# Kernel tuning notes

Hardware: AMD Instinct MI355X
Metric: run time of the kernel (lower is better)

Reference implementation:

```python
import jax, jax.numpy as jnp
import numpy as np

B, Lc, Le, H, V = 128, 512, 512, 512, 128
PAD_IDX = 0  # ignore_index for cross entropy


def _lstm_cell(x, h, c, Wih, Whh, bih, bhh):
    # PyTorch gate order: i, f, g, o
    gates = x @ Wih.T + h @ Whh.T + bih + bhh
    i, f, g, o = jnp.split(gates, 4, axis=-1)
    c_new = jax.nn.sigmoid(f) * c + jax.nn.sigmoid(i) * jnp.tanh(g)
    h_new = jax.nn.sigmoid(o) * jnp.tanh(c_new)
    return h_new, c_new


def setup_inputs() -> dict:
    key = jax.random.key(0)
    ks = jax.random.split(key, 16)
    s = 0.05  # weight init scale
    inp = {
        "C": jax.random.normal(ks[0], (B, Lc, V), jnp.float32),
        "C_pad": jax.random.randint(ks[1], (B, Lc), 0, 2, jnp.int32).at[:, 0].set(0),
        "E": jax.random.randint(ks[2], (B, Le), 0, V, jnp.int32),
        "E_emb": jax.random.normal(ks[3], (B, Le, V), jnp.float32),
        # encoder LSTM (input V -> hidden H)
        "enc_Wih": s * jax.random.normal(ks[4], (4 * H, V), jnp.float32),
        "enc_Whh": s * jax.random.normal(ks[5], (4 * H, H), jnp.float32),
        "enc_bih": jnp.zeros((4 * H,), jnp.float32),
        "enc_bhh": jnp.zeros((4 * H,), jnp.float32),
        # decoder LSTMCell (input V+H -> hidden H); input is concat([E_emb_t, V_prev])
        "dec_Wih": s * jax.random.normal(ks[6], (4 * H, V + H), jnp.float32),
        "dec_Whh": s * jax.random.normal(ks[7], (4 * H, H), jnp.float32),
        "dec_bih": jnp.zeros((4 * H,), jnp.float32),
        "dec_bhh": jnp.zeros((4 * H,), jnp.float32),
        # attention_proj: Linear(H, H, bias=False)
        "att_W": s * jax.random.normal(ks[8], (H, H), jnp.float32),
        # output_proj: Linear(2H, H)
        "out_W": s * jax.random.normal(ks[9], (H, 2 * H), jnp.float32),
        "out_b": jnp.zeros((H,), jnp.float32),
        # vocab_proj: Linear(H, V)
        "voc_W": s * jax.random.normal(ks[10], (V, H), jnp.float32),
        "voc_b": jnp.zeros((V,), jnp.float32),
    }
    return inp


def reference(C, C_pad, E, E_emb, enc_Wih, enc_Whh, enc_bih, enc_bhh,
              dec_Wih, dec_Whh, dec_bih, dec_bhh, att_W, out_W, out_b,
              voc_W, voc_b):
    Bv = C.shape[0]
    Hh = enc_Whh.shape[1]

    # ---- encoder LSTM over compressed input ----
    def enc_step(carry, x_t):
        h, c = carry
        h, c = _lstm_cell(x_t, h, c, enc_Wih, enc_Whh, enc_bih, enc_bhh)
        return (h, c), h

    h0 = jnp.zeros((Bv, Hh), C.dtype)
    (hT, cT), enc_hs = jax.lax.scan(enc_step, (h0, h0), jnp.swapaxes(C, 0, 1))
    enc_hs = jnp.swapaxes(enc_hs, 0, 1)  # (B, Lc, H)
    pad = C_pad.astype(bool)              # (B, Lc)

    # ---- decoder loop (training mode, teacher forcing) ----
    def dec_step(carry, e_t):
        h, c, Vprev = carry
        x = jnp.concatenate([e_t, Vprev], axis=1)  # (B, V+H)
        h, c = _lstm_cell(x, h, c, dec_Wih, dec_Whh, dec_bih, dec_bhh)
        q = h @ att_W.T                                    # (B, H)
        scores = jnp.einsum('blh,bh->bl', enc_hs, q)       # (B, Lc)
        scores = jnp.where(pad, -jnp.inf, scores)
        d = jax.nn.softmax(scores, axis=1)
        attn = jnp.einsum('bl,blh->bh', d, enc_hs)         # (B, H)
        U = jnp.concatenate([h, attn], axis=1)             # (B, 2H)
        Vnew = U @ out_W.T + out_b                         # (B, H)
        # dropout treated as identity (eval-mode determinism)
        logits = jnp.tanh(Vnew) @ voc_W.T + voc_b          # (B, V)
        return (h, c, Vnew), logits

    Vinit = jnp.zeros((Bv, Hh), C.dtype)
    _, logits = jax.lax.scan(dec_step, (hT, cT, Vinit),
                             jnp.swapaxes(E_emb[:, :-1], 0, 1))
    logits = jnp.swapaxes(logits, 0, 1)  # (B, Le-1, V)

    # ---- cross entropy with ignore_index=PAD_IDX ----
    targets = E[:, 1:].astype(jnp.int32)
    logp = jax.nn.log_softmax(logits, axis=-1)
    nll = -jnp.take_along_axis(logp, targets[..., None], axis=-1)[..., 0]
    mask = (targets != PAD_IDX).astype(nll.dtype)
    loss = jnp.sum(nll * mask) / jnp.maximum(jnp.sum(mask), 1.0)
    return loss
```

## Files before the change

kernel.cpp:

```cpp
#include <hip/hip_runtime.h>
#include <hip/hip_bf16.h>


#define NWG 256
#define NT  256

typedef unsigned short u16;
typedef unsigned int   u32;
typedef unsigned long long u64;
typedef __attribute__((ext_vector_type(4))) float f4;
typedef __attribute__((ext_vector_type(8))) short s8;

constexpr int Bv=128, Lc=512, Le=512, Hd=512, Vc=128;
constexpr int KE=640, KD=1152;
constexpr int CAP = 144;
constexpr int SPN = 24;

constexpr size_t O_WENC = 4096;
constexpr size_t O_WDEC = O_WENC + (size_t)2048*KE*2;
constexpr size_t O_WDF  = O_WDEC + (size_t)2048*KD*2;
constexpr size_t O_ATWT = O_WDF  + (size_t)2048*KD*2;
constexpr size_t O_OUTW = O_ATWT + (size_t)512*512*2;
constexpr size_t O_VOCW = O_OUTW + (size_t)512*1024*2;
constexpr size_t O_BE   = O_VOCW + (size_t)128*512*2;
constexpr size_t O_BD   = O_BE + 8192;
constexpr size_t O_BDF  = O_BD + 8192;
constexpr size_t O_H    = O_BDF + 8192;
constexpr size_t O_TNH  = O_H + (size_t)2*128*512*2;
constexpr size_t O_PFX  = O_TNH + (size_t)2*128*512*2;
constexpr size_t O_CNT  = O_PFX + (size_t)128*512*4;
constexpr size_t O_PMS  = O_CNT + 512;
constexpr size_t O_PACC = O_PMS + 2048;
constexpr size_t O_REC  = O_PACC + (size_t)256*512*2;
constexpr size_t O_LOSS = O_REC + (size_t)2*128*2*4*4;
constexpr size_t O_ENC  = O_LOSS + 256;
constexpr size_t O_PSP  = O_ENC + (size_t)128*512*512*2;

constexpr int SC       = CAP*1024;
constexpr int SM_BYTES = SC + 16384;

struct P {
  const float *C; const int *Cpad; const int *E; const float *Eemb;
  const float *eWih,*eWhh,*ebih,*ebhh;
  const float *dWih,*dWhh,*dbih,*dbhh;
  const float *attW,*outW,*outb,*vocW,*vocb;
  char* ws; float* out;
};

__device__ inline u16 f2bf(float x){
  u32 u = __float_as_uint(x);
  return (u16)((u + 0x7fffu + ((u>>16)&1u)) >> 16);
}
__device__ inline float bf2f(u16 b){ return __uint_as_float(((u32)b)<<16); }
__device__ inline float sigm(float x){ return 1.f/(1.f+expf(-x)); }
__device__ inline f4 MM(s8 a, s8 b, f4 c){
  return __builtin_amdgcn_mfma_f32_16x16x32_bf16(a, b, c, 0, 0, 0);
}
__device__ inline u64 ld64a(const void* p){
  return __hip_atomic_load((const u64*)p, __ATOMIC_RELAXED, __HIP_MEMORY_SCOPE_AGENT);
}
__device__ inline u32 ld32u(const void* p){
  return __hip_atomic_load((const u32*)p, __ATOMIC_RELAXED, __HIP_MEMORY_SCOPE_AGENT);
}
__device__ inline void st64a(void* p, u64 v){
  __hip_atomic_store((u64*)p, v, __ATOMIC_RELAXED, __HIP_MEMORY_SCOPE_AGENT);
}
__device__ inline void st32a(void* p, u32 v){
  __hip_atomic_store((u32*)p, v, __ATOMIC_RELAXED, __HIP_MEMORY_SCOPE_AGENT);
}
__device__ inline s8 ld16a(const void* p){
  union { u64 q[2]; s8 v; } u;
  u.q[0] = ld64a(p); u.q[1] = ld64a((const char*)p + 8);
  return u.v;
}
__device__ inline s8 cvt8(const float* p){
  f4 u = *(const f4*)p, v = *(const f4*)(p+4);
  s8 r;
  r[0]=(short)f2bf(u[0]); r[1]=(short)f2bf(u[1]); r[2]=(short)f2bf(u[2]); r[3]=(short)f2bf(u[3]);
  r[4]=(short)f2bf(v[0]); r[5]=(short)f2bf(v[1]); r[6]=(short)f2bf(v[2]); r[7]=(short)f2bf(v[3]);
  return r;
}
__device__ inline float wredmax(float v){
  #pragma unroll
  for (int m=32;m;m>>=1) v = fmaxf(v, __shfl_xor(v,m,64));
  return v;
}
__device__ inline float wredsum(float v){
  #pragma unroll
  for (int m=32;m;m>>=1) v += __shfl_xor(v,m,64);
  return v;
}

extern "C" __global__ void __launch_bounds__(NT,1) k_main(P p)
{
  extern __shared__ char sm[];
  const int wg = blockIdx.x, tid = threadIdx.x;
  const int gt = wg*NT + tid;
  const int rg = wg >> 5, cg = wg & 31;

  char* ws = p.ws;
  u32*  slotA = (u32*)ws;
  u32*  slotR = (u32*)(ws + 1024 + rg*128);
  u16*  wenc = (u16*)(ws + O_WENC);
  u16*  wdec = (u16*)(ws + O_WDEC);
  u16*  wdf  = (u16*)(ws + O_WDF);
  u16*  atwt = (u16*)(ws + O_ATWT);
  u16*  outw = (u16*)(ws + O_OUTW);
  u16*  vocw = (u16*)(ws + O_VOCW);
  float* be  = (float*)(ws + O_BE);
  float* bd  = (float*)(ws + O_BD);
  float* bdf = (float*)(ws + O_BDF);
  u16*  hbf  = (u16*)(ws + O_H);
  u16*  tnhb = (u16*)(ws + O_TNH);
  u32*  pfx  = (u32*)(ws + O_PFX);
  u32*  cntp = (u32*)(ws + O_CNT);
  u64*  pms  = (u64*)(ws + O_PMS);
  u16*  pacc16 = (u16*)(ws + O_PACC);
  float* rec = (float*)(ws + O_REC);
  float* losp= (float*)(ws + O_LOSS);
  u16*  encc = (u16*)(ws + O_ENC);
  u16*  spl  = (u16*)(ws + O_PSP) + (size_t)wg*SPN*Hd;

  u32 genA = 0, genG = 0;
  auto GBall = [&](){
    genA++;
    __syncthreads();
    if (tid == 0){
      __builtin_amdgcn_fence(__ATOMIC_RELEASE, "agent");
      st32a(slotA + wg, genA);
    }
    if (tid < 64){
      bool done = false;
      while (!done){
        u32 v0 = ld32u(slotA + tid);
        u32 v1 = ld32u(slotA + 64 + tid);
        u32 v2 = ld32u(slotA + 128 + tid);
        u32 v3 = ld32u(slotA + 192 + tid);
        done = __all((v0>=genA)&&(v1>=genA)&&(v2>=genA)&&(v3>=genA));
        if (!done) __builtin_amdgcn_s_sleep(4);
      }
      __builtin_amdgcn_fence(__ATOMIC_ACQUIRE, "agent");
    }
    __syncthreads();
  };
  auto RGB = [&](){
    genG++;
    __syncthreads();
    if (tid == 0) st32a(slotR + cg, genG);
    if (tid < 64){
      bool done = false;
      while (!done){
        u32 v = ld32u(slotR + (tid & 31));
        done = __all(v >= genG);
        if (!done) __builtin_amdgcn_s_sleep(2);
      }
      __builtin_amdgcn_fence(__ATOMIC_ACQUIRE, "workgroup");
    }
    __syncthreads();
  };

  for (int i = gt; i < 2048*KE; i += NWG*NT){
    int row = i / KE, k = i - row*KE;
    float v = (k < 128) ? p.eWih[row*128 + k] : p.eWhh[row*512 + (k-128)];
    wenc[i] = f2bf(v);
  }
  for (int i = gt; i < 2048*KD; i += NWG*NT){
    int row = i / KD, k = i - row*KD;
    float v = (k < 640) ? p.dWih[row*640 + k] : p.dWhh[row*512 + (k-640)];
    wdec[i] = f2bf(v);
  }
  for (int i = gt; i < 512*512;  i += NWG*NT){
    int kk = i >> 9, j = i & 511;
    atwt[i] = f2bf(p.attW[(size_t)j*512 + kk]);
  }
  for (int i = gt; i < 512*1024; i += NWG*NT) outw[i] = f2bf(p.outW[i]);
  for (int i = gt; i < 128*512;  i += NWG*NT) vocw[i] = f2bf(p.vocW[i]);
  for (int i = gt; i < 2048;     i += NWG*NT){ be[i] = p.ebih[i]+p.ebhh[i]; bd[i] = p.dbih[i]+p.dbhh[i]; }
  { u32* hz = (u32*)hbf; for (int i = gt; i < 65536; i += NWG*NT) hz[i] = 0; }
  if (gt == 0){ losp[0] = 0.f; losp[1] = 0.f; }

  {
    const int g0 = wg*8;
    float* dv = (float*)sm;
    for (int i = tid; i < 8*512; i += NT)
      dv[i] = p.dWih[(size_t)(g0 + (i>>9))*640 + 128 + (i&511)];
    __syncthreads();
    float wa[8][4];
    #pragma unroll
    for (int r=0;r<8;r++){ wa[r][0]=0;wa[r][1]=0;wa[r][2]=0;wa[r][3]=0; }
    for (int o = 0; o < 512; o++){
      float b0 = p.outW[(size_t)o*1024 + tid];
      float b1 = p.outW[(size_t)o*1024 + 256 + tid];
      float b2 = p.outW[(size_t)o*1024 + 512 + tid];
      float b3 = p.outW[(size_t)o*1024 + 768 + tid];
      #pragma unroll
      for (int r=0;r<8;r++){
        float d = dv[r*512+o];
        wa[r][0] += d*b0; wa[r][1] += d*b1; wa[r][2] += d*b2; wa[r][3] += d*b3;
      }
    }
    #pragma unroll
    for (int r=0;r<8;r++){
      int g = g0 + r;
      #pragma unroll
      for (int j=0;j<4;j++){
        int c = tid + 256*j;
        if (c < 512) wdf[(size_t)g*KD + 128 + c] = f2bf(p.dWhh[(size_t)g*512 + c] + wa[r][j]);
        else         wdf[(size_t)g*KD + 640 + (c-512)] = f2bf(wa[r][j]);
      }
    }
    for (int i = tid; i < 8*128; i += NT){
      int r = i >> 7, k = i & 127;
      wdf[(size_t)(g0+r)*KD + k] = f2bf(p.dWih[(size_t)(g0+r)*640 + k]);
    }
    if (tid < 8){
      int g = g0 + tid;
      float s = p.dbih[g] + p.dbhh[g];
      for (int o = 0; o < 512; o++) s += dv[tid*512+o]*p.outb[o];
      bdf[g] = s;
    }
    __syncthreads();
  }

  if (wg < 128){
    int* padl = (int*)(sm + SC);
    for (int i = tid; i < 512; i += NT) padl[i] = p.Cpad[wg*512 + i];
    __syncthreads();
    if (tid == 0){
      u32 run = 0;
      for (int tt = 0; tt < 512; tt++){ pfx[wg*512+tt] = run; if (padl[tt] == 0) run++; }
      cntp[wg] = run;
    }
    __syncthreads();
  }
  GBall();

  const int l  = tid & 63, wv = tid >> 6;
  const int n2 = wv >> 1, k2 = wv & 1;
  const int kl = (l>>4) << 3;
  const int ar = rg*16 + (l&15);
  float cst = 0.f;
  float accN = 0.f, accC = 0.f;

  const int rowA = rg*16 + (cg >> 1), halfA = cg & 1;
  const int cnA = (int)cntp[rowA], c2A = cnA >> 1;
  const int loA = halfA ? c2A : 0;
  const int mynA = (halfA ? cnA : c2A) - loA;
  const int ncapA = mynA < CAP ? mynA : CAP;
  const int limA  = mynA < CAP+SPN ? mynA : CAP+SPN;
  u16* eP = (u16*)sm;

  auto CEREC = [&](int tl){
    u32* th16 = (u32*)(sm + SC + 11776);
    float* lgp = (float*)(sm + SC + 12800);
    float* lgh = (float*)(sm + SC + 13824);
    const u16* tb = tnhb + (size_t)(tl&1)*Bv*Hd + (size_t)rowA*Hd;
    th16[tid] = ld32u(tb + 2*tid);
    __syncthreads();
    {
      int v = tid & 63, ksl = tid >> 6;
      int gv = halfA*64 + v;
      const u16* wp = vocw + (size_t)gv*Hd + ksl*128;
      const u16* hp = (const u16*)th16 + ksl*128;
      float acc = 0.f;
      #pragma unroll 4
      for (int j = 0; j < 16; j++){
        s8 wv8 = *(const s8*)(wp + j*8);
        #pragma unroll
        for (int q = 0; q < 8; q++) acc += bf2f((u16)wv8[q]) * bf2f(hp[j*8+q]);
      }
      lgp[ksl*64 + v] = acc;
    }
    __syncthreads();
    if (tid < 64){
      int gv = halfA*64 + tid;
      float lv = lgp[tid] + lgp[64+tid] + lgp[128+tid] + lgp[192+tid] + p.vocb[gv];
      lgh[tid] = lv;
      float m = wredmax(lv);
      float s = wredsum(expf(lv - m));
      if (tid == 0){
        int tgt = p.E[rowA*Le + tl + 1];
        float tlg = (tgt >= halfA*64 && tgt < halfA*64+64) ? lgh[tgt - halfA*64] : 0.f;
        float* rp = rec + ((size_t)(tl&1)*256 + rowA*2 + halfA)*4;
        union { u64 q; float f[2]; } pk; pk.f[0]=m; pk.f[1]=s;
        st64a(rp, pk.q);
        st32a(rp+2, __float_as_uint(tlg));
      }
    }
    __syncthreads();
  };
  auto COMB = [&](int tl){
    int tgt = p.E[rowA*Le + tl + 1];
    if (tgt != 0){
      const float* rp = rec + ((size_t)(tl&1)*256 + rowA*2)*4;
      union { u64 q; float f[2]; } a, b;
      a.q = ld64a(rp); b.q = ld64a(rp+4);
      float tA = __uint_as_float(ld32u(rp+2)), tB = __uint_as_float(ld32u(rp+6));
      float M = fmaxf(a.f[0], b.f[0]);
      float S = a.f[1]*expf(a.f[0]-M) + b.f[1]*expf(b.f[0]-M);
      accN += logf(S) + M - (tA + tB);
      accC += 1.f;
    }
  };

  const int gR0 = (n2*2+0)*512 + cg*16 + (l&15);
  const int gR1 = (n2*2+1)*512 + cg*16 + (l&15);

  for (int t = 0; t < Lc; t++){
    const u16* hold = hbf + (t&1)*Bv*Hd;
    u16* hnew       = hbf + ((t+1)&1)*Bv*Hd;
    s8 a[10];
    if (k2 == 0){
      #pragma unroll
      for (int ks = 4; ks < 10; ks++)
        a[ks] = ld16a(hold + (size_t)ar*Hd + (ks*32 + kl - 128));
      #pragma unroll
      for (int ks = 0; ks < 4; ks++)
        a[ks] = cvt8(p.C + ((size_t)ar*Lc + t)*Vc + ks*32 + kl);
    } else {
      #pragma unroll
      for (int ks = 0; ks < 10; ks++)
        a[ks] = ld16a(hold + (size_t)ar*Hd + (192 + ks*32 + kl));
    }
    f4 acc0 = {0,0,0,0}, acc1 = {0,0,0,0};
    #pragma unroll
    for (int ks = 0; ks < 10; ks++){
      int k = k2*320 + ks*32 + kl;
      acc0 = MM(a[ks], *(const s8*)(wenc + (size_t)gR0*KE + k), acc0);
      acc1 = MM(a[ks], *(const s8*)(wenc + (size_t)gR1*KE + k), acc1);
    }
    float* exch = (float*)(sm + SC);
    #pragma unroll
    for (int r = 0; r < 4; r++){
      int row = ((l>>4)<<2) + r;
      exch[((k2*4 + n2*2+0)*16 + row)*16 + (l&15)] = acc0[r];
      exch[((k2*4 + n2*2+1)*16 + row)*16 + (l&15)] = acc1[r];
    }
    __syncthreads();
    {
      int row = tid >> 4, u = tid & 15;
      int gb = cg*16 + u;
      float gi = exch[((0)*16+row)*16+u] + exch[((4)*16+row)*16+u] + be[0*512+gb];
      float gf = exch[((1)*16+row)*16+u] + exch[((5)*16+row)*16+u] + be[1*512+gb];
      float gg = exch[((2)*16+row)*16+u] + exch[((6)*16+row)*16+u] + be[2*512+gb];
      float go = exch[((3)*16+row)*16+u] + exch[((7)*16+row)*16+u] + be[3*512+gb];
      float fi = sigm(gi), ff = sigm(gf), fg = tanhf(gg), fo = sigm(go);
      cst = ff*cst + fi*fg;
      float hn = fo * tanhf(cst);
      int b = rg*16 + row;
      u32 hb = f2bf(hn);
      u32 nb = __shfl_xor((int)hb, 1, 64);
      if ((tid & 1) == 0){
        u32 pk = hb | (nb << 16);
        st32a(hnew + (size_t)b*Hd + gb, pk);
        if (p.Cpad[b*Lc + t] == 0){
          u32 pos = pfx[b*Lc + t];
          st32a(encc + ((size_t)b*Lc + pos)*Hd + gb, pk);
        }
      }
    }
    RGB();
  }

  GBall();

  {
    const u16* erow = encc + ((size_t)rowA*Lc + loA)*Hd;
    for (int it = 0; it*16 < limA; it++){
      s8 afr[16];
      const u16* ap = erow + (size_t)(it*16 + (l&15))*Hd;
      #pragma unroll
      for (int ks = 0; ks < 16; ks++) afr[ks] = *(const s8*)(ap + ks*32 + kl);
      for (int ot = 0; ot < 8; ot++){
        int kout0 = wv*128 + ot*16;
        f4 acc = {0,0,0,0};
        #pragma unroll
        for (int ks = 0; ks < 16; ks++)
          acc = MM(afr[ks], *(const s8*)(atwt + (size_t)(kout0 + (l&15))*Hd + ks*32 + kl), acc);
        #pragma unroll
        for (int r = 0; r < 4; r++){
          int prow = it*16 + ((l>>4)<<2) + r;
          int pcol = kout0 + (l&15);
          if (prow < limA){
            u16 pv = f2bf(acc[r]);
            if (prow < CAP) eP[(size_t)prow*Hd + pcol] = pv;
            else            spl[(size_t)(prow-CAP)*Hd + pcol] = pv;
          }
        }
      }
    }
    __syncthreads();
  }

  float* exch = (float*)(sm + SC);
  float* vex  = (float*)(sm + SC + 8192);
  float* sc2  = (float*)(sm + SC + 12288);
  s8 aH[14];

  for (int t = 0; t < Le-1; t++){
    const u16* hold = hbf + (t&1)*Bv*Hd;
    u16* hnew       = hbf + ((t+1)&1)*Bv*Hd;

    if (t == 0){
      s8 a[10];
      #pragma unroll
      for (int ks = 0; ks < 10; ks++){
        int ke = (k2==0) ? ((ks<4) ? ks*32+kl : 640 + (ks-4)*32 + kl)
                         : (832 + ks*32 + kl);
        if (ke < 128) a[ks] = cvt8(p.Eemb + ((size_t)ar*Le + 0)*Vc + ke);
        else          a[ks] = ld16a(hold + (size_t)ar*Hd + (ke-640));
      }
      f4 acc0 = {0,0,0,0}, acc1 = {0,0,0,0};
      #pragma unroll
      for (int ks = 0; ks < 10; ks++){
        int ke = (k2==0) ? ((ks<4) ? ks*32+kl : 640 + (ks-4)*32 + kl)
                         : (832 + ks*32 + kl);
        acc0 = MM(a[ks], *(const s8*)(wdec + (size_t)gR0*KD + ke), acc0);
        acc1 = MM(a[ks], *(const s8*)(wdec + (size_t)gR1*KD + ke), acc1);
      }
      #pragma unroll
      for (int r = 0; r < 4; r++){
        int row = ((l>>4)<<2) + r;
        exch[((k2*4 + n2*2+0)*16 + row)*16 + (l&15)] = acc0[r];
        exch[((k2*4 + n2*2+1)*16 + row)*16 + (l&15)] = acc1[r];
      }
      __syncthreads();
      {
        int row = tid >> 4, u = tid & 15;
        int gb = cg*16 + u;
        float gi = exch[((0)*16+row)*16+u] + exch[((4)*16+row)*16+u] + bd[0*512+gb];
        float gf = exch[((1)*16+row)*16+u] + exch[((5)*16+row)*16+u] + bd[1*512+gb];
        float gg = exch[((2)*16+row)*16+u] + exch[((6)*16+row)*16+u] + bd[2*512+gb];
        float go = exch[((3)*16+row)*16+u] + exch[((7)*16+row)*16+u] + bd[3*512+gb];
        float fi = sigm(gi), ff = sigm(gf), fg = tanhf(gg), fo = sigm(go);
        cst = ff*cst + fi*fg;
        float hn = fo * tanhf(cst);
        u32 hb = f2bf(hn);
        u32 nb = __shfl_xor((int)hb, 1, 64);
        if ((tid & 1) == 0)
          st32a(hnew + (size_t)(rg*16+row)*Hd + gb, hb | (nb << 16));
      }
    } else {
      if (tid < 16){
        union { u64 q; float f[2]; } uA, uB;
        uA.q = ld64a(pms + (rg*16+tid)*2 + 0);
        uB.q = ld64a(pms + (rg*16+tid)*2 + 1);
        float M = fmaxf(uA.f[0], uB.f[0]);
        float eA = (uA.f[0] > -1e29f) ? expf(uA.f[0]-M) : 0.f;
        float eB = (uB.f[0] > -1e29f) ? expf(uB.f[0]-M) : 0.f;
        float den = uA.f[1]*eA + uB.f[1]*eB;
        sc2[tid*2]   = eA/den;
        sc2[tid*2+1] = eB/den;
      }
      __syncthreads();
      const int colc = cg*16 + (l&15);
      if (k2 == 0){
        s8 a[18];
        #pragma unroll
        for (int ks = 4; ks < 18; ks++) a[ks] = aH[ks-4];
        #pragma unroll
        for (int ks = 0; ks < 4; ks++)
          a[ks] = cvt8(p.Eemb + ((size_t)ar*Le + t)*Vc + ks*32 + kl);
        f4 acc0 = {0,0,0,0}, acc1 = {0,0,0,0}, vac = {0,0,0,0};
        #pragma unroll
        for (int ks = 0; ks < 18; ks++){
          int k = ks*32 + kl;
          acc0 = MM(a[ks], *(const s8*)(wdf + (size_t)gR0*KD + k), acc0);
          acc1 = MM(a[ks], *(const s8*)(wdf + (size_t)gR1*KD + k), acc1);
          int ck = ks - 4;
          if (ck >= 0 && ((ck & 1) == n2))
            vac = MM(a[ks], *(const s8*)(outw + (size_t)colc*1024 + ck*32 + kl), vac);
        }
        #pragma unroll
        for (int r = 0; r < 4; r++){
          int row = ((l>>4)<<2) + r;
          exch[((n2*2+0)*16 + row)*16 + (l&15)] = acc0[r];
          exch[((n2*2+1)*16 + row)*16 + (l&15)] = acc1[r];
          vex[wv*256 + row*16 + (l&15)] = vac[r];
        }
      } else {
        const u16* pA = pacc16 + (size_t)(ar*2+0)*Hd;
        const u16* pB = pacc16 + (size_t)(ar*2+1)*Hd;
        s8 h0f = aH[0], h1f = aH[1];
        f4 acc0 = {0,0,0,0}, acc1 = {0,0,0,0};
        f4 aA0 = {0,0,0,0}, aA1 = {0,0,0,0}, aB0 = {0,0,0,0}, aB1 = {0,0,0,0};
        f4 vH = {0,0,0,0}, vA = {0,0,0,0}, vB = {0,0,0,0};
        acc0 = MM(h0f, *(const s8*)(wdf + (size_t)gR0*KD + 576 + kl), acc0);
        acc1 = MM(h0f, *(const s8*)(wdf + (size_t)gR1*KD + 576 + kl), acc1);
        acc0 = MM(h1f, *(const s8*)(wdf + (size_t)gR0*KD + 608 + kl), acc0);
        acc1 = MM(h1f, *(const s8*)(wdf + (size_t)gR1*KD + 608 + kl), acc1);
        {
          s8 hf = (n2 == 0) ? h0f : h1f;
          vH = MM(hf, *(const s8*)(outw + (size_t)colc*1024 + (14+n2)*32 + kl), vH);
        }
        #pragma unroll
        for (int hb = 0; hb < 2; hb++){
          s8 pf[8];
          #pragma unroll
          for (int j = 0; j < 8; j++)
            pf[j] = ld16a(pA + (hb*8+j)*32 + kl);
          #pragma unroll
          for (int j = 0; j < 8; j++){
            int c = hb*8 + j;
            int k = 640 + c*32 + kl;
            aA0 = MM(pf[j], *(const s8*)(wdf + (size_t)gR0*KD + k), aA0);
            aA1 = MM(pf[j], *(const s8*)(wdf + (size_t)gR1*KD + k), aA1);
            if (((16 + c) & 1) == n2)
              vA = MM(pf[j], *(const s8*)(outw + (size_t)colc*1024 + (16+c)*32 + kl), vA);
          }
        }
        #pragma unroll
        for (int hb = 0; hb < 2; hb++){
          s8 pf[8];
          #pragma unroll
          for (int j = 0; j < 8; j++)
            pf[j] = ld16a(pB + (hb*8+j)*32 + kl);
          #pragma unroll
          for (int j = 0; j < 8; j++){
            int c = hb*8 + j;
            int k = 640 + c*32 + kl;
            aB0 = MM(pf[j], *(const s8*)(wdf + (size_t)gR0*KD + k), aB0);
            aB1 = MM(pf[j], *(const s8*)(wdf + (size_t)gR1*KD + k), aB1);
            if (((16 + c) & 1) == n2)
              vB = MM(pf[j], *(const s8*)(outw + (size_t)colc*1024 + (16+c)*32 + kl), vB);
          }
        }
        #pragma unroll
        for (int r = 0; r < 4; r++){
          int row = ((l>>4)<<2) + r;
          float sAr = sc2[row*2], sBr = sc2[row*2+1];
          exch[((4 + n2*2+0)*16 + row)*16 + (l&15)] = acc0[r] + sAr*aA0[r] + sBr*aB0[r];
          exch[((4 + n2*2+1)*16 + row)*16 + (l&15)] = acc1[r] + sAr*aA1[r] + sBr*aB1[r];
          vex[wv*256 + row*16 + (l&15)] = vH[r] + sAr*vA[r] + sBr*vB[r];
        }
      }
      __syncthreads();
      {
        int row = tid >> 4, u = tid & 15;
        int gb = cg*16 + u;
        float gi = exch[((0)*16+row)*16+u] + exch[((4)*16+row)*16+u] + bdf[0*512+gb];
        float gf = exch[((1)*16+row)*16+u] + exch[((5)*16+row)*16+u] + bdf[1*512+gb];
        float gg = exch[((2)*16+row)*16+u] + exch[((6)*16+row)*16+u] + bdf[2*512+gb];
        float go = exch[((3)*16+row)*16+u] + exch[((7)*16+row)*16+u] + bdf[3*512+gb];
        float fi = sigm(gi), ff = sigm(gf), fg = tanhf(gg), fo = sigm(go);
        cst = ff*cst + fi*fg;
        float hn = fo * tanhf(cst);
        u32 hb = f2bf(hn);
        u32 nb = __shfl_xor((int)hb, 1, 64);
        if ((tid & 1) == 0)
          st32a(hnew + (size_t)(rg*16+row)*Hd + gb, hb | (nb << 16));
        float v = vex[row*16+u] + vex[256+row*16+u] + vex[512+row*16+u]
                + vex[768+row*16+u] + p.outb[gb];
        u32 tb2 = f2bf(tanhf(v));
        u32 tn2 = __shfl_xor((int)tb2, 1, 64);
        if ((tid & 1) == 0){
          u16* tnw = tnhb + (size_t)((t-1)&1)*Bv*Hd;
          st32a(tnw + (size_t)(rg*16+row)*Hd + gb, tb2 | (tn2 << 16));
        }
      }
    }
    RGB();

    {
      const int ne = limA, ncap = ncapA;
      float* hld = (float*)(sm + SC);
      float* scl = (float*)(sm + SC + 2048);
      float* red = (float*)(sm + SC + 2816);
      float* part= (float*)(sm + SC + 3584);
      {
        u32 hw = ld32u(hnew + (size_t)rowA*Hd + 2*tid);
        int c0 = 2*tid, c1 = c0+1;
        hld[(c0&15)*32 + (c0>>4)] = bf2f((u16)(hw & 0xffffu));
        hld[(c1&15)*32 + (c1>>4)] = bf2f((u16)(hw >> 16));
      }
      __syncthreads();
      const int pg8 = tid >> 5, ln = tid & 31;
      int i = pg8;
      for (; i < ncap; i += 8){
        const u16* e = eP + (size_t)i*Hd + ln*16;
        s8 ev0 = *(const s8*)(e);
        s8 ev1 = *(const s8*)(e+8);
        float s = 0.f;
        #pragma unroll
        for (int j=0;j<8;j++) s += bf2f((u16)ev0[j]) * hld[j*32+ln];
        #pragma unroll
        for (int j=0;j<8;j++) s += bf2f((u16)ev1[j]) * hld[(j+8)*32+ln];
        #pragma unroll
        for (int m=1;m<32;m<<=1) s += __shfl_xor(s, m, 64);
        if (ln == 0) scl[i] = s;
      }
      for (; i < ne; i += 8){
        const u16* e = spl + (size_t)(i-CAP)*Hd + ln*16;
        s8 ev0 = *(const s8*)(e);
        s8 ev1 = *(const s8*)(e+8);
        float s = 0.f;
        #pragma unroll
        for (int j=0;j<8;j++) s += bf2f((u16)ev0[j]) * hld[j*32+ln];
        #pragma unroll
        for (int j=0;j<8;j++) s += bf2f((u16)ev1[j]) * hld[(j+8)*32+ln];
        #pragma unroll
        for (int m=1;m<32;m<<=1) s += __shfl_xor(s, m, 64);
        if (ln == 0) scl[i] = s;
      }
      __syncthreads();
      float mloc = -1e30f;
      for (int i2 = tid; i2 < ne; i2 += NT) mloc = fmaxf(mloc, scl[i2]);
      mloc = wredmax(mloc);
      if ((tid&63)==0) red[tid>>6] = mloc;
      __syncthreads();
      float M = fmaxf(fmaxf(red[0],red[1]), fmaxf(red[2],red[3]));
      __syncthreads();
      float sloc = 0.f;
      for (int i2 = tid; i2 < ne; i2 += NT){ float w = expf(scl[i2]-M); scl[i2]=w; sloc += w; }
      sloc = wredsum(sloc);
      if ((tid&63)==0) red[tid>>6] = sloc;
      __syncthreads();
      float S = red[0]+red[1]+red[2]+red[3];
      float a8[8] = {0,0,0,0,0,0,0,0};
      const u16* eb2 = encc + ((size_t)rowA*Lc + loA)*Hd + l*8;
      int ii = wv;
      for (; ii + 12 < ne; ii += 16){
        s8 e0 = *(const s8*)(eb2 + (size_t)(ii   )*Hd);
        s8 e1 = *(const s8*)(eb2 + (size_t)(ii+ 4)*Hd);
        s8 e2 = *(const s8*)(eb2 + (size_t)(ii+ 8)*Hd);
        s8 e3 = *(const s8*)(eb2 + (size_t)(ii+12)*Hd);
        float w0=scl[ii], w1=scl[ii+4], w2=scl[ii+8], w3=scl[ii+12];
        #pragma unroll
        for (int j=0;j<8;j++) a8[j] += w0*bf2f((u16)e0[j]);
        #pragma unroll
        for (int j=0;j<8;j++) a8[j] += w1*bf2f((u16)e1[j]);
        #pragma unroll
        for (int j=0;j<8;j++) a8[j] += w2*bf2f((u16)e2[j]);
        #pragma unroll
        for (int j=0;j<8;j++) a8[j] += w3*bf2f((u16)e3[j]);
      }
      for (; ii < ne; ii += 4){
        s8 e0 = *(const s8*)(eb2 + (size_t)ii*Hd);
        float w0 = scl[ii];
        #pragma unroll
        for (int j=0;j<8;j++) a8[j] += w0*bf2f((u16)e0[j]);
      }
      { f4 v0 = {a8[0],a8[1],a8[2],a8[3]}, v1 = {a8[4],a8[5],a8[6],a8[7]};
        *(f4*)(part + wv*512 + l*8)     = v0;
        *(f4*)(part + wv*512 + l*8 + 4) = v1; }
      __syncthreads();
      {
        int h0 = 2*tid;
        float a0 = part[h0] + part[512+h0] + part[1024+h0] + part[1536+h0];
        float a1 = part[h0+1] + part[512+h0+1] + part[1024+h0+1] + part[1536+h0+1];
        st32a(pacc16 + (size_t)(rowA*2+halfA)*Hd + h0, (u32)f2bf(a0) | ((u32)f2bf(a1) << 16));
        if (tid == 0){
          union { u64 q; float f[2]; } pk; pk.f[0]=M; pk.f[1]=S;
          st64a(pms + rowA*2 + halfA, pk.q);
        }
      }
      __syncthreads();
      if (t >= 1) CEREC(t-1);
      if (t >= 2 && halfA == 0 && tid == 0) COMB(t-2);
      if (t < Le-2){
        if (k2 == 0){
          #pragma unroll
          for (int ks = 4; ks < 18; ks++)
            aH[ks-4] = ld16a(hnew + (size_t)ar*Hd + (ks*32 + kl - 128));
        } else {
          aH[0] = ld16a(hnew + (size_t)ar*Hd + (448 + kl));
          aH[1] = ld16a(hnew + (size_t)ar*Hd + (480 + kl));
        }
      }
    }
    RGB();
  }

  const int TL = Le-2;
  {
    if (tid < 16){
      union { u64 q; float f[2]; } uA, uB;
      uA.q = ld64a(pms + (rg*16+tid)*2 + 0);
      uB.q = ld64a(pms + (rg*16+tid)*2 + 1);
      float M = fmaxf(uA.f[0], uB.f[0]);
      float eA = (uA.f[0] > -1e29f) ? expf(uA.f[0]-M) : 0.f;
      float eB = (uB.f[0] > -1e29f) ? expf(uB.f[0]-M) : 0.f;
      float den = uA.f[1]*eA + uB.f[1]*eB;
      sc2[tid*2]   = eA/den;
      sc2[tid*2+1] = eB/den;
    }
    __syncthreads();
    const float scA = sc2[(l&15)*2], scB = sc2[(l&15)*2+1];
    const u16* h5 = hbf + (size_t)((TL+1)&1)*Bv*Hd;
    const u16* pA = pacc16 + (size_t)(ar*2+0)*Hd;
    const u16* pB = pacc16 + (size_t)(ar*2+1)*Hd;
    const int colc = cg*16 + (l&15);
    f4 vac = {0,0,0,0};
    #pragma unroll
    for (int j = 0; j < 8; j++){
      int kv = k2*16 + j*2 + n2;
      s8 af;
      if (kv < 16) af = ld16a(h5 + (size_t)ar*Hd + kv*32 + kl);
      else {
        s8 va = ld16a(pA + (kv-16)*32 + kl);
        s8 vb = ld16a(pB + (kv-16)*32 + kl);
        #pragma unroll
        for (int q = 0; q < 8; q++)
          af[q] = (short)f2bf(scA*bf2f((u16)va[q]) + scB*bf2f((u16)vb[q]));
      }
      vac = MM(af, *(const s8*)(outw + (size_t)colc*1024 + kv*32 + kl), vac);
    }
    #pragma unroll
    for (int r = 0; r < 4; r++)
      vex[wv*256 + (((l>>4)<<2)+r)*16 + (l&15)] = vac[r];
    __syncthreads();
    {
      int row = tid >> 4, u = tid & 15;
      int gb = cg*16 + u;
      float v = vex[row*16+u] + vex[256+row*16+u] + vex[512+row*16+u]
              + vex[768+row*16+u] + p.outb[gb];
      u32 tb2 = f2bf(tanhf(v));
      u32 tn2 = __shfl_xor((int)tb2, 1, 64);
      if ((tid & 1) == 0){
        u16* tnw = tnhb + (size_t)(TL&1)*Bv*Hd;
        st32a(tnw + (size_t)(rg*16+row)*Hd + gb, tb2 | (tn2 << 16));
      }
    }
  }
  RGB();
  {
    CEREC(TL);
    if (halfA == 0 && tid == 0) COMB(TL-1);
  }
  RGB();
  {
    if (halfA == 0 && tid == 0){
      COMB(TL);
      atomicAdd(losp + 0, accN);
      atomicAdd(losp + 1, accC);
    }
  }
  GBall();
  if (wg == 0 && tid == 0) p.out[0] = losp[0] / fmaxf(losp[1], 1.f);
}

extern "C" void kernel_launch(void* const* d_in, const int* in_sizes, int n_in,
                              void* d_out, int out_size, void* d_ws, size_t ws_size,
                              hipStream_t stream)
{
  hipFuncSetAttribute(reinterpret_cast<const void*>(k_main),
                      hipFuncAttributeMaxDynamicSharedMemorySize, SM_BYTES);
  hipMemsetAsync(d_ws, 0, 4096, stream);

  P prm;
  prm.C    = (const float*)d_in[0];
  prm.Cpad = (const int*)  d_in[1];
  prm.E    = (const int*)  d_in[2];
  prm.Eemb = (const float*)d_in[3];
  prm.eWih = (const float*)d_in[4];
  prm.eWhh = (const float*)d_in[5];
  prm.ebih = (const float*)d_in[6];
  prm.ebhh = (const float*)d_in[7];
  prm.dWih = (const float*)d_in[8];
  prm.dWhh = (const float*)d_in[9];
  prm.dbih = (const float*)d_in[10];
  prm.dbhh = (const float*)d_in[11];
  prm.attW = (const float*)d_in[12];
  prm.outW = (const float*)d_in[13];
  prm.outb = (const float*)d_in[14];
  prm.vocW = (const float*)d_in[15];
  prm.vocb = (const float*)d_in[16];
  prm.ws   = (char*)d_ws;
  prm.out  = (float*)d_out;

  k_main<<<dim3(NWG), dim3(NT), SM_BYTES, stream>>>(prm);
}
```

Before: 21.57 ms.

## Double threads per workgroup to 512 and split per-wave MFMA work

Raises the workgroup size from 256 to 512 threads, so each wave now computes one gate tile instead of two, and the attention, vocab and output-projection reductions are split across 8 waves instead of 4. The encoder cache capacity in shared memory shrinks slightly to make room for larger exchange buffers. The aim is to shorten the serial per-timestep critical path of the persistent recurrent kernel by spreading MFMA and memory work over more waves. In exchange it adds more cross-wave reduction, leaves half the threads idle in the elementwise phases, and may raise register pressure per CU.

Measured after the change: 25.82 ms. +19.8%, slower.

```diff
diff --git a/kernel.cpp b/kernel.cpp
--- a/kernel.cpp
+++ b/kernel.cpp
@@ -3,7 +3,7 @@
 
 
 #define NWG 256
-#define NT  256
+#define NT  512
 
 typedef unsigned short u16;
 typedef unsigned int   u32;
@@ -13,7 +13,7 @@
 
 constexpr int Bv=128, Lc=512, Le=512, Hd=512, Vc=128;
 constexpr int KE=640, KD=1152;
-constexpr int CAP = 144;
+constexpr int CAP = 140;
 constexpr int SPN = 24;
 
 constexpr size_t O_WENC = 4096;
@@ -37,7 +37,7 @@
 constexpr size_t O_PSP  = O_ENC + (size_t)128*512*512*2;
 
 constexpr int SC       = CAP*1024;
-constexpr int SM_BYTES = SC + 16384;
+constexpr int SM_BYTES = SC + 20480;
 
 struct P {
   const float *C; const int *Cpad; const int *E; const float *Eemb;
@@ -185,26 +185,24 @@
     for (int i = tid; i < 8*512; i += NT)
       dv[i] = p.dWih[(size_t)(g0 + (i>>9))*640 + 128 + (i&511)];
     __syncthreads();
-    float wa[8][4];
+    float wa[8][2];
     #pragma unroll
-    for (int r=0;r<8;r++){ wa[r][0]=0;wa[r][1]=0;wa[r][2]=0;wa[r][3]=0; }
+    for (int r=0;r<8;r++){ wa[r][0]=0; wa[r][1]=0; }
     for (int o = 0; o < 512; o++){
       float b0 = p.outW[(size_t)o*1024 + tid];
-      float b1 = p.outW[(size_t)o*1024 + 256 + tid];
-      float b2 = p.outW[(size_t)o*1024 + 512 + tid];
-      float b3 = p.outW[(size_t)o*1024 + 768 + tid];
+      float b1 = p.outW[(size_t)o*1024 + 512 + tid];
       #pragma unroll
       for (int r=0;r<8;r++){
         float d = dv[r*512+o];
-        wa[r][0] += d*b0; wa[r][1] += d*b1; wa[r][2] += d*b2; wa[r][3] += d*b3;
+        wa[r][0] += d*b0; wa[r][1] += d*b1;
       }
     }
     #pragma unroll
     for (int r=0;r<8;r++){
       int g = g0 + r;
       #pragma unroll
-      for (int j=0;j<4;j++){
-        int c = tid + 256*j;
+      for (int j=0;j<2;j++){
+        int c = tid + 512*j;
         if (c < 512) wdf[(size_t)g*KD + 128 + c] = f2bf(p.dWhh[(size_t)g*512 + c] + wa[r][j]);
         else         wdf[(size_t)g*KD + 640 + (c-512)] = f2bf(wa[r][j]);
       }
@@ -236,7 +234,7 @@
   GBall();
 
   const int l  = tid & 63, wv = tid >> 6;
-  const int n2 = wv >> 1, k2 = wv & 1;
+  const int ct = wv >> 1, kh = wv & 1;
   const int kl = (l>>4) << 3;
   const int ar = rg*16 + (l&15);
   float cst = 0.f;
@@ -251,20 +249,20 @@
   u16* eP = (u16*)sm;
 
   auto CEREC = [&](int tl){
-    u32* th16 = (u32*)(sm + SC + 11776);
-    float* lgp = (float*)(sm + SC + 12800);
-    float* lgh = (float*)(sm + SC + 13824);
+    u32* th16 = (u32*)(sm + SC);
+    float* lgp = (float*)(sm + SC + 1024);
+    float* lgh = (float*)(sm + SC + 3072);
     const u16* tb = tnhb + (size_t)(tl&1)*Bv*Hd + (size_t)rowA*Hd;
-    th16[tid] = ld32u(tb + 2*tid);
+    if (tid < 256) th16[tid] = ld32u(tb + 2*tid);
     __syncthreads();
     {
       int v = tid & 63, ksl = tid >> 6;
       int gv = halfA*64 + v;
-      const u16* wp = vocw + (size_t)gv*Hd + ksl*128;
-      const u16* hp = (const u16*)th16 + ksl*128;
+      const u16* wp = vocw + (size_t)gv*Hd + ksl*64;
+      const u16* hp = (const u16*)th16 + ksl*64;
       float acc = 0.f;
-      #pragma unroll 4
-      for (int j = 0; j < 16; j++){
+      #pragma unroll
+      for (int j = 0; j < 8; j++){
         s8 wv8 = *(const s8*)(wp + j*8);
         #pragma unroll
         for (int q = 0; q < 8; q++) acc += bf2f((u16)wv8[q]) * bf2f(hp[j*8+q]);
@@ -274,7 +272,9 @@
     __syncthreads();
     if (tid < 64){
       int gv = halfA*64 + tid;
-      float lv = lgp[tid] + lgp[64+tid] + lgp[128+tid] + lgp[192+tid] + p.vocb[gv];
+      float lv = p.vocb[gv];
+      #pragma unroll
+      for (int s2 = 0; s2 < 8; s2++) lv += lgp[s2*64+tid];
       lgh[tid] = lv;
       float m = wredmax(lv);
       float s = wredsum(expf(lv - m));
@@ -303,14 +303,13 @@
     }
   };
 
-  const int gR0 = (n2*2+0)*512 + cg*16 + (l&15);
-  const int gR1 = (n2*2+1)*512 + cg*16 + (l&15);
+  const int gRt = ct*512 + cg*16 + (l&15);
 
   for (int t = 0; t < Lc; t++){
     const u16* hold = hbf + (t&1)*Bv*Hd;
     u16* hnew       = hbf + ((t+1)&1)*Bv*Hd;
     s8 a[10];
-    if (k2 == 0){
+    if (kh == 0){
       #pragma unroll
       for (int ks = 4; ks < 10; ks++)
         a[ks] = ld16a(hold + (size_t)ar*Hd + (ks*32 + kl - 128));
@@ -322,22 +321,20 @@
       for (int ks = 0; ks < 10; ks++)
         a[ks] = ld16a(hold + (size_t)ar*Hd + (192 + ks*32 + kl));
     }
-    f4 acc0 = {0,0,0,0}, acc1 = {0,0,0,0};
+    f4 acc = {0,0,0,0};
     #pragma unroll
     for (int ks = 0; ks < 10; ks++){
-      int k = k2*320 + ks*32 + kl;
-      acc0 = MM(a[ks], *(const s8*)(wenc + (size_t)gR0*KE + k), acc0);
-      acc1 = MM(a[ks], *(const s8*)(wenc + (size_t)gR1*KE + k), acc1);
+      int k = kh*320 + ks*32 + kl;
+      acc = MM(a[ks], *(const s8*)(wenc + (size_t)gRt*KE + k), acc);
     }
     float* exch = (float*)(sm + SC);
     #pragma unroll
     for (int r = 0; r < 4; r++){
       int row = ((l>>4)<<2) + r;
-      exch[((k2*4 + n2*2+0)*16 + row)*16 + (l&15)] = acc0[r];
-      exch[((k2*4 + n2*2+1)*16 + row)*16 + (l&15)] = acc1[r];
-    }
-    __syncthreads();
-    {
+      exch[((kh*4 + ct)*16 + row)*16 + (l&15)] = acc[r];
+    }
+    __syncthreads();
+    if (tid < 256){
       int row = tid >> 4, u = tid & 15;
       int gb = cg*16 + u;
       float gi = exch[((0)*16+row)*16+u] + exch[((4)*16+row)*16+u] + be[0*512+gb];
@@ -371,8 +368,8 @@
       const u16* ap = erow + (size_t)(it*16 + (l&15))*Hd;
       #pragma unroll
       for (int ks = 0; ks < 16; ks++) afr[ks] = *(const s8*)(ap + ks*32 + kl);
-      for (int ot = 0; ot < 8; ot++){
-        int kout0 = wv*128 + ot*16;
+      for (int ot = 0; ot < 4; ot++){
+        int kout0 = wv*64 + ot*16;
         f4 acc = {0,0,0,0};
         #pragma unroll
         for (int ks = 0; ks < 16; ks++)
@@ -394,7 +391,7 @@
 
   float* exch = (float*)(sm + SC);
   float* vex  = (float*)(sm + SC + 8192);
-  float* sc2  = (float*)(sm + SC + 12288);
+  float* sc2  = (float*)(sm + SC + 16384);
   s8 aH[14];
 
   for (int t = 0; t < Le-1; t++){
@@ -405,27 +402,25 @@
       s8 a[10];
       #pragma unroll
       for (int ks = 0; ks < 10; ks++){
-        int ke = (k2==0) ? ((ks<4) ? ks*32+kl : 640 + (ks-4)*32 + kl)
+        int ke = (kh==0) ? ((ks<4) ? ks*32+kl : 640 + (ks-4)*32 + kl)
                          : (832 + ks*32 + kl);
         if (ke < 128) a[ks] = cvt8(p.Eemb + ((size_t)ar*Le + 0)*Vc + ke);
         else          a[ks] = ld16a(hold + (size_t)ar*Hd + (ke-640));
       }
-      f4 acc0 = {0,0,0,0}, acc1 = {0,0,0,0};
+      f4 acc = {0,0,0,0};
       #pragma unroll
       for (int ks = 0; ks < 10; ks++){
-        int ke = (k2==0) ? ((ks<4) ? ks*32+kl : 640 + (ks-4)*32 + kl)
+        int ke = (kh==0) ? ((ks<4) ? ks*32+kl : 640 + (ks-4)*32 + kl)
                          : (832 + ks*32 + kl);
-        acc0 = MM(a[ks], *(const s8*)(wdec + (size_t)gR0*KD + ke), acc0);
-        acc1 = MM(a[ks], *(const s8*)(wdec + (size_t)gR1*KD + ke), acc1);
+        acc = MM(a[ks], *(const s8*)(wdec + (size_t)gRt*KD + ke), acc);
       }
       #pragma unroll
       for (int r = 0; r < 4; r++){
         int row = ((l>>4)<<2) + r;
-        exch[((k2*4 + n2*2+0)*16 + row)*16 + (l&15)] = acc0[r];
-        exch[((k2*4 + n2*2+1)*16 + row)*16 + (l&15)] = acc1[r];
-      }
-      __syncthreads();
-      {
+        exch[((kh*4 + ct)*16 + row)*16 + (l&15)] = acc[r];
+      }
+      __syncthreads();
+      if (tid < 256){
         int row = tid >> 4, u = tid & 15;
         int gb = cg*16 + u;
         float gi = exch[((0)*16+row)*16+u] + exch[((4)*16+row)*16+u] + bd[0*512+gb];
@@ -454,44 +449,40 @@
       }
       __syncthreads();
       const int colc = cg*16 + (l&15);
-      if (k2 == 0){
+      if (kh == 0){
         s8 a[18];
         #pragma unroll
         for (int ks = 4; ks < 18; ks++) a[ks] = aH[ks-4];
         #pragma unroll
         for (int ks = 0; ks < 4; ks++)
           a[ks] = cvt8(p.Eemb + ((size_t)ar*Le + t)*Vc + ks*32 + kl);
-        f4 acc0 = {0,0,0,0}, acc1 = {0,0,0,0}, vac = {0,0,0,0};
+        f4 acc = {0,0,0,0}, vac = {0,0,0,0};
         #pragma unroll
         for (int ks = 0; ks < 18; ks++){
           int k = ks*32 + kl;
-          acc0 = MM(a[ks], *(const s8*)(wdf + (size_t)gR0*KD + k), acc0);
-          acc1 = MM(a[ks], *(const s8*)(wdf + (size_t)gR1*KD + k), acc1);
+          acc = MM(a[ks], *(const s8*)(wdf + (size_t)gRt*KD + k), acc);
           int ck = ks - 4;
-          if (ck >= 0 && ((ck & 1) == n2))
+          if (ck >= ct*4 && ck < ct*4+4 && ck < 14)
             vac = MM(a[ks], *(const s8*)(outw + (size_t)colc*1024 + ck*32 + kl), vac);
         }
         #pragma unroll
         for (int r = 0; r < 4; r++){
           int row = ((l>>4)<<2) + r;
-          exch[((n2*2+0)*16 + row)*16 + (l&15)] = acc0[r];
-          exch[((n2*2+1)*16 + row)*16 + (l&15)] = acc1[r];
+          exch[((ct)*16 + row)*16 + (l&15)] = acc[r];
           vex[wv*256 + row*16 + (l&15)] = vac[r];
         }
       } else {
         const u16* pA = pacc16 + (size_t)(ar*2+0)*Hd;
         const u16* pB = pacc16 + (size_t)(ar*2+1)*Hd;
         s8 h0f = aH[0], h1f = aH[1];
-        f4 acc0 = {0,0,0,0}, acc1 = {0,0,0,0};
-        f4 aA0 = {0,0,0,0}, aA1 = {0,0,0,0}, aB0 = {0,0,0,0}, aB1 = {0,0,0,0};
+        f4 acc = {0,0,0,0};
+        f4 aA = {0,0,0,0}, aB = {0,0,0,0};
         f4 vH = {0,0,0,0}, vA = {0,0,0,0}, vB = {0,0,0,0};
-        acc0 = MM(h0f, *(const s8*)(wdf + (size_t)gR0*KD + 576 + kl), acc0);
-        acc1 = MM(h0f, *(const s8*)(wdf + (size_t)gR1*KD + 576 + kl), acc1);
-        acc0 = MM(h1f, *(const s8*)(wdf + (size_t)gR0*KD + 608 + kl), acc0);
-        acc1 = MM(h1f, *(const s8*)(wdf + (size_t)gR1*KD + 608 + kl), acc1);
-        {
-          s8 hf = (n2 == 0) ? h0f : h1f;
-          vH = MM(hf, *(const s8*)(outw + (size_t)colc*1024 + (14+n2)*32 + kl), vH);
+        acc = MM(h0f, *(const s8*)(wdf + (size_t)gRt*KD + 576 + kl), acc);
+        acc = MM(h1f, *(const s8*)(wdf + (size_t)gRt*KD + 608 + kl), acc);
+        if (ct == 0){
+          vH = MM(h0f, *(const s8*)(outw + (size_t)colc*1024 + 14*32 + kl), vH);
+          vH = MM(h1f, *(const s8*)(outw + (size_t)colc*1024 + 15*32 + kl), vH);
         }
         #pragma unroll
         for (int hb = 0; hb < 2; hb++){
@@ -503,9 +494,8 @@
           for (int j = 0; j < 8; j++){
             int c = hb*8 + j;
             int k = 640 + c*32 + kl;
-            aA0 = MM(pf[j], *(const s8*)(wdf + (size_t)gR0*KD + k), aA0);
-            aA1 = MM(pf[j], *(const s8*)(wdf + (size_t)gR1*KD + k), aA1);
-            if (((16 + c) & 1) == n2)
+            aA = MM(pf[j], *(const s8*)(wdf + (size_t)gRt*KD + k), aA);
+            if (c >= ct*4 && c < ct*4+4)
               vA = MM(pf[j], *(const s8*)(outw + (size_t)colc*1024 + (16+c)*32 + kl), vA);
           }
         }
@@ -519,9 +509,8 @@
           for (int j = 0; j < 8; j++){
             int c = hb*8 + j;
             int k = 640 + c*32 + kl;
-            aB0 = MM(pf[j], *(const s8*)(wdf + (size_t)gR0*KD + k), aB0);
-            aB1 = MM(pf[j], *(const s8*)(wdf + (size_t)gR1*KD + k), aB1);
-            if (((16 + c) & 1) == n2)
+            aB = MM(pf[j], *(const s8*)(wdf + (size_t)gRt*KD + k), aB);
+            if (c >= ct*4 && c < ct*4+4)
               vB = MM(pf[j], *(const s8*)(outw + (size_t)colc*1024 + (16+c)*32 + kl), vB);
           }
         }
@@ -529,13 +518,12 @@
         for (int r = 0; r < 4; r++){
           int row = ((l>>4)<<2) + r;
           float sAr = sc2[row*2], sBr = sc2[row*2+1];
-          exch[((4 + n2*2+0)*16 + row)*16 + (l&15)] = acc0[r] + sAr*aA0[r] + sBr*aB0[r];
-          exch[((4 + n2*2+1)*16 + row)*16 + (l&15)] = acc1[r] + sAr*aA1[r] + sBr*aB1[r];
+          exch[((4 + ct)*16 + row)*16 + (l&15)] = acc[r] + sAr*aA[r] + sBr*aB[r];
           vex[wv*256 + row*16 + (l&15)] = vH[r] + sAr*vA[r] + sBr*vB[r];
         }
       }
       __syncthreads();
-      {
+      if (tid < 256){
         int row = tid >> 4, u = tid & 15;
         int gb = cg*16 + u;
         float gi = exch[((0)*16+row)*16+u] + exch[((4)*16+row)*16+u] + bdf[0*512+gb];
@@ -549,8 +537,9 @@
         u32 nb = __shfl_xor((int)hb, 1, 64);
         if ((tid & 1) == 0)
           st32a(hnew + (size_t)(rg*16+row)*Hd + gb, hb | (nb << 16));
-        float v = vex[row*16+u] + vex[256+row*16+u] + vex[512+row*16+u]
-                + vex[768+row*16+u] + p.outb[gb];
+        float v = p.outb[gb];
+        #pragma unroll
+        for (int w2 = 0; w2 < 8; w2++) v += vex[w2*256 + row*16 + u];
         u32 tb2 = f2bf(tanhf(v));
         u32 tn2 = __shfl_xor((int)tb2, 1, 64);
         if ((tid & 1) == 0){
@@ -567,16 +556,16 @@
       float* scl = (float*)(sm + SC + 2048);
       float* red = (float*)(sm + SC + 2816);
       float* part= (float*)(sm + SC + 3584);
-      {
+      if (tid < 256){
         u32 hw = ld32u(hnew + (size_t)rowA*Hd + 2*tid);
         int c0 = 2*tid, c1 = c0+1;
         hld[(c0&15)*32 + (c0>>4)] = bf2f((u16)(hw & 0xffffu));
         hld[(c1&15)*32 + (c1>>4)] = bf2f((u16)(hw >> 16));
       }
       __syncthreads();
-      const int pg8 = tid >> 5, ln = tid & 31;
-      int i = pg8;
-      for (; i < ncap; i += 8){
+      const int sub = tid >> 5, ln = tid & 31;
+      int i = sub;
+      for (; i < ncap; i += 16){
         const u16* e = eP + (size_t)i*Hd + ln*16;
         s8 ev0 = *(const s8*)(e);
         s8 ev1 = *(const s8*)(e+8);
@@ -589,7 +578,7 @@
         for (int m=1;m<32;m<<=1) s += __shfl_xor(s, m, 64);
         if (ln == 0) scl[i] = s;
       }
-      for (; i < ne; i += 8){
+      for (; i < ne; i += 16){
         const u16* e = spl + (size_t)(i-CAP)*Hd + ln*16;
         s8 ev0 = *(const s8*)(e);
         s8 ev1 = *(const s8*)(e+8);
@@ -608,23 +597,27 @@
       mloc = wredmax(mloc);
       if ((tid&63)==0) red[tid>>6] = mloc;
       __syncthreads();
-      float M = fmaxf(fmaxf(red[0],red[1]), fmaxf(red[2],red[3]));
+      float M = -1e30f;
+      #pragma unroll
+      for (int w2 = 0; w2 < 8; w2++) M = fmaxf(M, red[w2]);
       __syncthreads();
       float sloc = 0.f;
       for (int i2 = tid; i2 < ne; i2 += NT){ float w = expf(scl[i2]-M); scl[i2]=w; sloc += w; }
       sloc = wredsum(sloc);
       if ((tid&63)==0) red[tid>>6] = sloc;
       __syncthreads();
-      float S = red[0]+red[1]+red[2]+red[3];
+      float S = 0.f;
+      #pragma unroll
+      for (int w2 = 0; w2 < 8; w2++) S += red[w2];
       float a8[8] = {0,0,0,0,0,0,0,0};
       const u16* eb2 = encc + ((size_t)rowA*Lc + loA)*Hd + l*8;
       int ii = wv;
-      for (; ii + 12 < ne; ii += 16){
-        s8 e0 = *(const s8*)(eb2 + (size_t)(ii   )*Hd);
-        s8 e1 = *(const s8*)(eb2 + (size_t)(ii+ 4)*Hd);
-        s8 e2 = *(const s8*)(eb2 + (size_t)(ii+ 8)*Hd);
-        s8 e3 = *(const s8*)(eb2 + (size_t)(ii+12)*Hd);
-        float w0=scl[ii], w1=scl[ii+4], w2=scl[ii+8], w3=scl[ii+12];
+      for (; ii + 24 < ne; ii += 32){
+        s8 e0 = *(const s8*)(eb2 + (size_t)(ii    )*Hd);
+        s8 e1 = *(const s8*)(eb2 + (size_t)(ii+ 8)*Hd);
+        s8 e2 = *(const s8*)(eb2 + (size_t)(ii+16)*Hd);
+        s8 e3 = *(const s8*)(eb2 + (size_t)(ii+24)*Hd);
+        float w0=scl[ii], w1=scl[ii+8], w2=scl[ii+16], w3=scl[ii+24];
         #pragma unroll
         for (int j=0;j<8;j++) a8[j] += w0*bf2f((u16)e0[j]);
         #pragma unroll
@@ -634,7 +627,7 @@
         #pragma unroll
         for (int j=0;j<8;j++) a8[j] += w3*bf2f((u16)e3[j]);
       }
-      for (; ii < ne; ii += 4){
+      for (; ii < ne; ii += 8){
         s8 e0 = *(const s8*)(eb2 + (size_t)ii*Hd);
         float w0 = scl[ii];
         #pragma unroll
@@ -644,10 +637,14 @@
         *(f4*)(part + wv*512 + l*8)     = v0;
         *(f4*)(part + wv*512 + l*8 + 4) = v1; }
       __syncthreads();
-      {
+      if (tid < 256){
         int h0 = 2*tid;
-        float a0 = part[h0] + part[512+h0] + part[1024+h0] + part[1536+h0];
-        float a1 = part[h0+1] + part[512+h0+1] + part[1024+h0+1] + part[1536+h0+1];
+        float a0 = 0.f, a1 = 0.f;
+        #pragma unroll
+        for (int w2 = 0; w2 < 8; w2++){
+          a0 += part[w2*512 + h0];
+          a1 += part[w2*512 + h0 + 1];
+        }
         st32a(pacc16 + (size_t)(rowA*2+halfA)*Hd + h0, (u32)f2bf(a0) | ((u32)f2bf(a1) << 16));
         if (tid == 0){
           union { u64 q; float f[2]; } pk; pk.f[0]=M; pk.f[1]=S;
@@ -658,7 +655,7 @@
       if (t >= 1) CEREC(t-1);
       if (t >= 2 && halfA == 0 && tid == 0) COMB(t-2);
       if (t < Le-2){
-        if (k2 == 0){
+        if (kh == 0){
           #pragma unroll
           for (int ks = 4; ks < 18; ks++)
             aH[ks-4] = ld16a(hnew + (size_t)ar*Hd + (ks*32 + kl - 128));
@@ -692,8 +689,8 @@
     const int colc = cg*16 + (l&15);
     f4 vac = {0,0,0,0};
     #pragma unroll
-    for (int j = 0; j < 8; j++){
-      int kv = k2*16 + j*2 + n2;
+    for (int j = 0; j < 4; j++){
+      int kv = wv*4 + j;
       s8 af;
       if (kv < 16) af = ld16a(h5 + (size_t)ar*Hd + kv*32 + kl);
       else {
@@ -709,11 +706,12 @@
     for (int r = 0; r < 4; r++)
       vex[wv*256 + (((l>>4)<<2)+r)*16 + (l&15)] = vac[r];
     __syncthreads();
-    {
+    if (tid < 256){
       int row = tid >> 4, u = tid & 15;
       int gb = cg*16 + u;
-      float v = vex[row*16+u] + vex[256+row*16+u] + vex[512+row*16+u]
-              + vex[768+row*16+u] + p.outb[gb];
+      float v = p.outb[gb];
+      #pragma unroll
+      for (int w2 = 0; w2 < 8; w2++) v += vex[w2*256 + row*16 + u];
       u32 tb2 = f2bf(tanhf(v));
       u32 tn2 = __shfl_xor((int)tb2, 1, 64);
       if ((tid & 1) == 0){
```
